# Performance work log

Measured on AMD Instinct MI355X. Metric: run time of the kernel, lower is better.

Reference implementation:

```python
import jax, jax.numpy as jnp
import numpy as np

EMBED_DIM = 768
NUM_HEADS = 12
HEAD_DIM = EMBED_DIM // NUM_HEADS
HIDDEN_DIM = int(EMBED_DIM * 4.0)
LN_EPS = 1e-5


def setup_inputs() -> dict:
    key = jax.random.key(0)
    ks = jax.random.split(key, 8)
    B, N, C = 16, 1024, EMBED_DIM
    s = 0.02
    return {
        "x": jax.random.normal(ks[0], (B, N, C), dtype=jnp.float32),
        "ln1_g": jnp.ones((C,), jnp.float32),
        "ln1_b": jnp.zeros((C,), jnp.float32),
        "qkv_w": jax.random.normal(ks[1], (C, 3 * C), jnp.float32) * s,
        "qkv_b": jnp.zeros((3 * C,), jnp.float32),
        "proj_w": jax.random.normal(ks[2], (C, C), jnp.float32) * s,
        "proj_b": jnp.zeros((C,), jnp.float32),
        "ln2_g": jnp.ones((C,), jnp.float32),
        "ln2_b": jnp.zeros((C,), jnp.float32),
        "fc1_w": jax.random.normal(ks[3], (C, HIDDEN_DIM), jnp.float32) * s,
        "fc1_b": jnp.zeros((HIDDEN_DIM,), jnp.float32),
        "fc2_w": jax.random.normal(ks[4], (HIDDEN_DIM, C), jnp.float32) * s,
        "fc2_b": jnp.zeros((C,), jnp.float32),
    }


def _layernorm(x, g, b):
    mu = jnp.mean(x, axis=-1, keepdims=True)
    var = jnp.mean(jnp.square(x - mu), axis=-1, keepdims=True)
    return (x - mu) * jax.lax.rsqrt(var + LN_EPS) * g + b


def _attention(x, qkv_w, qkv_b, proj_w, proj_b):
    B, N, C = x.shape
    qkv = x @ qkv_w + qkv_b                       # [B,N,3C]
    qkv = qkv.reshape(B, N, 3, NUM_HEADS, HEAD_DIM)
    q, k, v = qkv[:, :, 0], qkv[:, :, 1], qkv[:, :, 2]  # [B,N,H,D]
    scale = HEAD_DIM ** -0.5
    attn = jnp.einsum("bqhd,bkhd->bhqk", q, k) * scale
    attn = jax.nn.softmax(attn, axis=-1)
    out = jnp.einsum("bhqk,bkhd->bqhd", attn, v).reshape(B, N, C)
    return out @ proj_w + proj_b


def reference(x, ln1_g, ln1_b, qkv_w, qkv_b, proj_w, proj_b,
              ln2_g, ln2_b, fc1_w, fc1_b, fc2_w, fc2_b):
    x = x + _attention(_layernorm(x, ln1_g, ln1_b), qkv_w, qkv_b, proj_w, proj_b)
    h = _layernorm(x, ln2_g, ln2_b)
    h = jax.nn.gelu(h @ fc1_w + fc1_b, approximate=False)
    return x + (h @ fc2_w + fc2_b)
```

## Files before the change

kernel.cpp:

```cpp
#include <hip/hip_runtime.h>
#include <math.h>

#define SEQ 1024
#define NH 12
#define CC 768

using short8 = __attribute__((ext_vector_type(8))) short;
using bf16x8 = __attribute__((ext_vector_type(8))) __bf16;
using f32x4  = __attribute__((ext_vector_type(4))) float;

__device__ __forceinline__ unsigned short f2bf(float f){
  unsigned u = __builtin_bit_cast(unsigned, f);
  u += 0x7FFF + ((u >> 16) & 1);
  return (unsigned short)(u >> 16);
}

__device__ __forceinline__ void gload16(const void* g, void* l){
  __builtin_amdgcn_global_load_lds((const __attribute__((address_space(1))) unsigned int*)g,
                                   (__attribute__((address_space(3))) unsigned int*)l, 16, 0, 0);
}
__device__ __forceinline__ bf16x8 lds_frag(const unsigned short* p){
  return __builtin_bit_cast(bf16x8, *(const short8*)p);
}
__device__ __forceinline__ bf16x8 gld_frag(const unsigned short* p){
  return __builtin_bit_cast(bf16x8, *(const short8*)p);
}

__global__ __launch_bounds__(256) void wtrans(const float* __restrict__ W,
                                              unsigned short* __restrict__ Wt,
                                              int K, int N){
  __shared__ float tile[32][33];
  int tx = threadIdx.x & 31, ty = threadIdx.x >> 5;
  int n0 = blockIdx.x * 32, k0 = blockIdx.y * 32;
#pragma unroll
  for (int j = 0; j < 4; j++)
    tile[ty + j*8][tx] = W[(size_t)(k0 + ty + j*8) * N + n0 + tx];
  __syncthreads();
#pragma unroll
  for (int j = 0; j < 4; j++)
    Wt[(size_t)(n0 + ty + j*8) * K + k0 + tx] = f2bf(tile[tx][ty + j*8]);
}

__global__ __launch_bounds__(64) void ln_k(const float* __restrict__ x,
                                           const float* __restrict__ g,
                                           const float* __restrict__ be,
                                           unsigned short* __restrict__ out){
  const int row = blockIdx.x;
  const int lane = threadIdx.x;
  const float* xr = x + (size_t)row * CC;
  float4 v[3];
  float s = 0.f, sq = 0.f;
#pragma unroll
  for (int j = 0; j < 3; j++){
    v[j] = *(const float4*)(xr + lane*4 + j*256);
    s  += v[j].x + v[j].y + v[j].z + v[j].w;
    sq += v[j].x*v[j].x + v[j].y*v[j].y + v[j].z*v[j].z + v[j].w*v[j].w;
  }
#pragma unroll
  for (int d = 1; d < 64; d <<= 1){ s += __shfl_xor(s, d); sq += __shfl_xor(sq, d); }
  float mu = s * (1.0f/CC);
  float var = sq * (1.0f/CC) - mu*mu;
  float rstd = rsqrtf(var + 1e-5f);
  unsigned short* orow = out + (size_t)row * CC;
#pragma unroll
  for (int j = 0; j < 3; j++){
    int cb = lane*4 + j*256;
    float4 gv = *(const float4*)(g + cb);
    float4 bv = *(const float4*)(be + cb);
    ushort4 o;
    o.x = f2bf((v[j].x - mu)*rstd*gv.x + bv.x);
    o.y = f2bf((v[j].y - mu)*rstd*gv.y + bv.y);
    o.z = f2bf((v[j].z - mu)*rstd*gv.z + bv.z);
    o.w = f2bf((v[j].w - mu)*rstd*gv.w + bv.w);
    *(ushort4*)(orow + cb) = o;
  }
}

__global__ __launch_bounds__(256) void vextract(const unsigned short* __restrict__ qkv,
                                                unsigned short* __restrict__ vT){
  __shared__ unsigned short tile[32][33];
  int bh = blockIdx.y;
  int b = bh / NH, h = bh % NH;
  int tt = blockIdx.x & 31, dt = blockIdx.x >> 5;
  int tx = threadIdx.x & 31, ty = threadIdx.x >> 5;
#pragma unroll
  for (int j = 0; j < 4; j++)
    tile[ty + j*8][tx] = qkv[(size_t)(b*SEQ + tt*32 + ty + j*8)*2304 + 1536 + h*64 + dt*32 + tx];
  __syncthreads();
#pragma unroll
  for (int j = 0; j < 4; j++)
    vT[((size_t)bh*64 + dt*32 + ty + j*8)*SEQ + tt*32 + tx] = tile[tx][ty + j*8];
}

template<int MODE>
__global__ __launch_bounds__(256, 2) void gemm_bt(const unsigned short* __restrict__ A,
                                                  const unsigned short* __restrict__ Bt,
                                                  const float* __restrict__ bias,
                                                  const float* __restrict__ resid,
                                                  void* __restrict__ outp,
                                                  int M, int N, int K){
  __shared__ __align__(16) unsigned short As[2][128*32];
  __shared__ __align__(16) unsigned short Bs[2][128*32];
  const int t = threadIdx.x;
  const int lane = t & 63;
  const int w = t >> 6;
  const int wr = w >> 1, wc = w & 1;
  const int l15 = lane & 15, lg = lane >> 4;
  const int mtiles = M >> 7;
  const int bm = blockIdx.x % mtiles;
  const int bn = blockIdx.x / mtiles;
  const unsigned short* Abase = A + (size_t)bm * 128 * K;
  const unsigned short* Bbase = Bt + (size_t)bn * 128 * K;

  f32x4 acc[4][4] = {};
  const int nk = K >> 5;
  int buf = 0;

#pragma unroll
  for (int i = 0; i < 2; i++){
    int idx = i*256 + t; int r = idx >> 2; int s = idx & 3; int ss = s ^ ((r >> 1) & 3);
    gload16(Abase + (size_t)r*K + ss*8, &As[0][idx*8]);
  }
#pragma unroll
  for (int i = 0; i < 2; i++){
    int idx = i*256 + t; int r = idx >> 2; int s = idx & 3; int ss = s ^ ((r >> 1) & 3);
    gload16(Bbase + (size_t)r*K + ss*8, &Bs[0][idx*8]);
  }
  __syncthreads();

  for (int kt = 0; kt < nk; ++kt){
    if (kt + 1 < nk){
      const unsigned short* Ak = Abase + (kt + 1) * 32;
      const unsigned short* Bk = Bbase + (kt + 1) * 32;
#pragma unroll
      for (int i = 0; i < 2; i++){
        int idx = i*256 + t; int r = idx >> 2; int s = idx & 3; int ss = s ^ ((r >> 1) & 3);
        gload16(Ak + (size_t)r*K + ss*8, &As[buf^1][idx*8]);
      }
#pragma unroll
      for (int i = 0; i < 2; i++){
        int idx = i*256 + t; int r = idx >> 2; int s = idx & 3; int ss = s ^ ((r >> 1) & 3);
        gload16(Bk + (size_t)r*K + ss*8, &Bs[buf^1][idx*8]);
      }
    }
    bf16x8 af[4], bfr[4];
#pragma unroll
    for (int m = 0; m < 4; m++){
      int rr = wr*64 + m*16 + l15;
      int s = lg ^ ((rr >> 1) & 3);
      af[m] = lds_frag(&As[buf][rr*32 + s*8]);
    }
#pragma unroll
    for (int n = 0; n < 4; n++){
      int rr = wc*64 + n*16 + l15;
      int s = lg ^ ((rr >> 1) & 3);
      bfr[n] = lds_frag(&Bs[buf][rr*32 + s*8]);
    }
#pragma unroll
    for (int m = 0; m < 4; m++)
#pragma unroll
      for (int n = 0; n < 4; n++)
        acc[m][n] = __builtin_amdgcn_mfma_f32_16x16x32_bf16(af[m], bfr[n], acc[m][n], 0, 0, 0);
    __syncthreads();
    buf ^= 1;
  }

  const int row0 = bm*128 + wr*64 + lg*4;
  const int col0 = bn*128 + wc*64 + l15;
#pragma unroll
  for (int n = 0; n < 4; n++){
    int c = col0 + n*16;
    float bv = bias[c];
#pragma unroll
    for (int m = 0; m < 4; m++){
      int r = row0 + m*16;
#pragma unroll
      for (int i = 0; i < 4; i++){
        size_t idx = (size_t)(r + i) * N + c;
        float v = acc[m][n][i] + bv;
        if constexpr (MODE == 0){
          ((unsigned short*)outp)[idx] = f2bf(v);
        } else if constexpr (MODE == 1){
          ((float*)outp)[idx] = resid[idx] + v;
        } else {
          float gv = 0.5f * v * (1.0f + erff(v * 0.70710678118654752440f));
          ((unsigned short*)outp)[idx] = f2bf(gv);
        }
      }
    }
  }
}

__global__ __launch_bounds__(256, 2) void attn_k(const unsigned short* __restrict__ qkv,
                                                 const unsigned short* __restrict__ vT,
                                                 unsigned short* __restrict__ aout){
  __shared__ __align__(16) unsigned short Ks[2][64*64];
  __shared__ __align__(16) unsigned short Vs[2][64*64];
  __shared__ __align__(16) unsigned short Ps[4][32*64];
  const int t = threadIdx.x, lane = t & 63, w = t >> 6;
  const int l15 = lane & 15, lg = lane >> 4;
  const int qt = blockIdx.x;
  const int bh = blockIdx.y;
  const int b = bh / NH, h = bh % NH;
  const size_t qrow0 = (size_t)b * SEQ + qt*128 + w*32;

  bf16x8 qf[2][2];
#pragma unroll
  for (int nf = 0; nf < 2; nf++)
#pragma unroll
    for (int ks = 0; ks < 2; ks++)
      qf[nf][ks] = gld_frag(qkv + (qrow0 + nf*16 + l15)*2304 + h*64 + ks*32 + lg*8);

  f32x4 o[2][4] = {};
  float mold[2] = {-3.0e38f, -3.0e38f};
  float lsum[2] = {0.f, 0.f};

  const unsigned short* Kgl = qkv + (size_t)b * SEQ * 2304 + 768 + h*64;
  const unsigned short* Vgl = vT + (size_t)bh * 64 * SEQ;

  auto stageKV = [&](int bufi, int kt){
#pragma unroll
    for (int i = 0; i < 2; i++){
      int idx = i*256 + t; int r = idx >> 3; int s = idx & 7; int ss = s ^ (r & 7);
      gload16(Kgl + (size_t)(kt*64 + r)*2304 + ss*8, &Ks[bufi][idx*8]);
    }
#pragma unroll
    for (int i = 0; i < 2; i++){
      int idx = i*256 + t; int r = idx >> 3; int s = idx & 7; int ss = s ^ (r & 7);
      gload16(Vgl + (size_t)r*SEQ + kt*64 + ss*8, &Vs[bufi][idx*8]);
    }
  };

  stageKV(0, 0);
  __syncthreads();
  int buf = 0;

  for (int kt = 0; kt < 16; ++kt){
    if (kt + 1 < 16) stageKV(buf ^ 1, kt + 1);

    f32x4 st[4][2] = {};
#pragma unroll
    for (int ks = 0; ks < 2; ks++){
      bf16x8 kf[4];
#pragma unroll
      for (int mf = 0; mf < 4; mf++){
        int rr = mf*16 + l15;
        int sc = (ks*4 + lg) ^ (rr & 7);
        kf[mf] = lds_frag(&Ks[buf][rr*64 + sc*8]);
      }
#pragma unroll
      for (int mf = 0; mf < 4; mf++)
#pragma unroll
        for (int nf = 0; nf < 2; nf++)
          st[mf][nf] = __builtin_amdgcn_mfma_f32_16x16x32_bf16(kf[mf], qf[nf][ks], st[mf][nf], 0, 0, 0);
    }

    float fsc[2];
#pragma unroll
    for (int nf = 0; nf < 2; nf++){
      float mx = -3.0e38f;
#pragma unroll
      for (int mf = 0; mf < 4; mf++)
#pragma unroll
        for (int i = 0; i < 4; i++){
          float sv = st[mf][nf][i] * 0.125f;
          st[mf][nf][i] = sv;
          mx = fmaxf(mx, sv);
        }
      mx = fmaxf(mx, __shfl_xor(mx, 16));
      mx = fmaxf(mx, __shfl_xor(mx, 32));
      float nm = fmaxf(mold[nf], mx);
      float f = __expf(mold[nf] - nm);
      mold[nf] = nm;
      float rs = 0.f;
#pragma unroll
      for (int mf = 0; mf < 4; mf++)
#pragma unroll
        for (int i = 0; i < 4; i++){
          float p = __expf(st[mf][nf][i] - nm);
          st[mf][nf][i] = p;
          rs += p;
        }
      rs += __shfl_xor(rs, 16);
      rs += __shfl_xor(rs, 32);
      lsum[nf] = lsum[nf]*f + rs;
      fsc[nf] = f;
    }

#pragma unroll
    for (int nf = 0; nf < 2; nf++)
#pragma unroll
      for (int mf = 0; mf < 4; mf++)
#pragma unroll
        for (int i = 0; i < 4; i++){
          int rP = nf*16 + l15;
          int col = mf*16 + lg*4 + i;
          Ps[w][rP*64 + (col ^ ((rP & 7) << 3))] = f2bf(st[mf][nf][i]);
        }

#pragma unroll
    for (int mm = 0; mm < 2; mm++)
#pragma unroll
      for (int i = 0; i < 4; i++){
        float fo = __shfl(fsc[mm], lg*4 + i);
#pragma unroll
        for (int df = 0; df < 4; df++)
          o[mm][df][i] *= fo;
      }

#pragma unroll
    for (int ks = 0; ks < 2; ks++){
      bf16x8 pf[2], vf[4];
#pragma unroll
      for (int mm = 0; mm < 2; mm++){
        int rP = mm*16 + l15;
        int sc = (ks*4 + lg) ^ (rP & 7);
        pf[mm] = lds_frag(&Ps[w][rP*64 + sc*8]);
      }
#pragma unroll
      for (int df = 0; df < 4; df++){
        int rr = df*16 + l15;
        int sc = (ks*4 + lg) ^ (rr & 7);
        vf[df] = lds_frag(&Vs[buf][rr*64 + sc*8]);
      }
#pragma unroll
      for (int mm = 0; mm < 2; mm++)
#pragma unroll
        for (int df = 0; df < 4; df++)
          o[mm][df] = __builtin_amdgcn_mfma_f32_16x16x32_bf16(pf[mm], vf[df], o[mm][df], 0, 0, 0);
    }
    __syncthreads();
    buf ^= 1;
  }

#pragma unroll
  for (int mm = 0; mm < 2; mm++){
    float li = 1.0f / lsum[mm];
#pragma unroll
    for (int i = 0; i < 4; i++){
      float rl = __shfl(li, lg*4 + i);
      size_t r = qrow0 + mm*16 + lg*4 + i;
#pragma unroll
      for (int df = 0; df < 4; df++)
        aout[r*CC + h*64 + df*16 + l15] = f2bf(o[mm][df][i] * rl);
    }
  }
}

extern "C" void kernel_launch(void* const* d_in, const int* in_sizes, int n_in,
                              void* d_out, int out_size, void* d_ws, size_t ws_size,
                              hipStream_t stream){
  (void)in_sizes; (void)n_in; (void)out_size; (void)ws_size;
  const float* x      = (const float*)d_in[0];
  const float* ln1_g  = (const float*)d_in[1];
  const float* ln1_b  = (const float*)d_in[2];
  const float* qkv_w  = (const float*)d_in[3];
  const float* qkv_b  = (const float*)d_in[4];
  const float* proj_w = (const float*)d_in[5];
  const float* proj_b = (const float*)d_in[6];
  const float* ln2_g  = (const float*)d_in[7];
  const float* ln2_b  = (const float*)d_in[8];
  const float* fc1_w  = (const float*)d_in[9];
  const float* fc1_b  = (const float*)d_in[10];
  const float* fc2_w  = (const float*)d_in[11];
  const float* fc2_b  = (const float*)d_in[12];
  float* out = (float*)d_out;
  char* ws = (char*)d_ws;

  unsigned short* ln_out  = (unsigned short*)(ws);
  unsigned short* qkv_buf = (unsigned short*)(ws + 25165824);
  unsigned short* vTb     = (unsigned short*)(ws + 100663296);
  unsigned short* attn    = (unsigned short*)(ws + 125829120);
  unsigned short* hbuf    = qkv_buf;
  char* wbase = ws + 150994944;
  unsigned short* wq = (unsigned short*)(wbase);
  unsigned short* wp = (unsigned short*)(wbase + 3538944);
  unsigned short* w1 = (unsigned short*)(wbase + 4718592);
  unsigned short* w2 = (unsigned short*)(wbase + 9437184);

  wtrans<<<dim3(72, 24), 256, 0, stream>>>(qkv_w, wq, 768, 2304);
  wtrans<<<dim3(24, 24), 256, 0, stream>>>(proj_w, wp, 768, 768);
  wtrans<<<dim3(96, 24), 256, 0, stream>>>(fc1_w, w1, 768, 3072);
  wtrans<<<dim3(24, 96), 256, 0, stream>>>(fc2_w, w2, 3072, 768);

  ln_k<<<16384, 64, 0, stream>>>(x, ln1_g, ln1_b, ln_out);
  gemm_bt<0><<<128*18, 256, 0, stream>>>(ln_out, wq, qkv_b, nullptr, qkv_buf, 16384, 2304, 768);
  vextract<<<dim3(64, 192), 256, 0, stream>>>(qkv_buf, vTb);
  attn_k<<<dim3(8, 192), 256, 0, stream>>>(qkv_buf, vTb, attn);
  gemm_bt<1><<<128*6, 256, 0, stream>>>(attn, wp, proj_b, x, out, 16384, 768, 768);
  ln_k<<<16384, 64, 0, stream>>>(out, ln2_g, ln2_b, ln_out);
  gemm_bt<2><<<128*24, 256, 0, stream>>>(ln_out, w1, fc1_b, nullptr, hbuf, 16384, 3072, 768);
  gemm_bt<1><<<128*6, 256, 0, stream>>>(hbuf, w2, fc2_b, out, out, 16384, 768, 3072);
}
```

Baseline: 625.4 us.

## Replace GEMM with 256x256-tile 8-wave pipelined kernel and tanh-based GELU

```diff
diff --git a/kernel.cpp b/kernel.cpp
--- a/kernel.cpp
+++ b/kernel.cpp
@@ -93,86 +93,157 @@
 }
 
 template<int MODE>
-__global__ __launch_bounds__(256, 2) void gemm_bt(const unsigned short* __restrict__ A,
+__global__ __launch_bounds__(512, 2) void gemm256(const unsigned short* __restrict__ A,
                                                   const unsigned short* __restrict__ Bt,
                                                   const float* __restrict__ bias,
                                                   const float* __restrict__ resid,
                                                   void* __restrict__ outp,
                                                   int M, int N, int K){
-  __shared__ __align__(16) unsigned short As[2][128*32];
-  __shared__ __align__(16) unsigned short Bs[2][128*32];
+  __shared__ __align__(16) unsigned short lds[2][4][128*64];
   const int t = threadIdx.x;
-  const int lane = t & 63;
-  const int w = t >> 6;
-  const int wr = w >> 1, wc = w & 1;
+  const int lane = t & 63, w = t >> 6;
+  const int wr = w >> 2, wc = w & 3;
   const int l15 = lane & 15, lg = lane >> 4;
-  const int mtiles = M >> 7;
-  const int bm = blockIdx.x % mtiles;
-  const int bn = blockIdx.x / mtiles;
-  const unsigned short* Abase = A + (size_t)bm * 128 * K;
-  const unsigned short* Bbase = Bt + (size_t)bn * 128 * K;
-
-  f32x4 acc[4][4] = {};
-  const int nk = K >> 5;
-  int buf = 0;
-
-#pragma unroll
-  for (int i = 0; i < 2; i++){
-    int idx = i*256 + t; int r = idx >> 2; int s = idx & 3; int ss = s ^ ((r >> 1) & 3);
-    gload16(Abase + (size_t)r*K + ss*8, &As[0][idx*8]);
-  }
-#pragma unroll
-  for (int i = 0; i < 2; i++){
-    int idx = i*256 + t; int r = idx >> 2; int s = idx & 3; int ss = s ^ ((r >> 1) & 3);
-    gload16(Bbase + (size_t)r*K + ss*8, &Bs[0][idx*8]);
-  }
-  __syncthreads();
-
+  const int mtiles = M >> 8;
+  const int cpx = gridDim.x >> 3;
+  const int bid = blockIdx.x;
+  const int swz = (bid & 7) * cpx + (bid >> 3);
+  const int bm = swz % mtiles, bn = swz / mtiles;
+
+  const unsigned short* gA0 = A  + (size_t)bm*256*K;
+  const unsigned short* gA1 = gA0 + (size_t)128*K;
+  const unsigned short* gB0 = Bt + (size_t)bn*256*K;
+  const unsigned short* gB1 = gB0 + (size_t)128*K;
+
+  const int csw = (t & 7) ^ ((t >> 3) & 7);
+  const size_t off0 = (size_t)(t >> 3)*K + csw*8;
+  const size_t off1 = off0 + (size_t)64*K;
+
+  auto stageh = [&](int bi, int rg, const unsigned short* gb, int kt){
+    const unsigned short* s = gb + (size_t)kt*64;
+    unsigned short* d = &lds[bi][rg][0];
+    gload16(s + off0, d + t*8);
+    gload16(s + off1, d + 4096 + t*8);
+  };
+
+  const int cx0 = (lg ^ (l15 & 7)) * 8;
+  const int cx1 = ((4 + lg) ^ (l15 & 7)) * 8;
+  const int rB = (wc & 1)*64 + l15;
+
+  f32x4 acc[8][4] = {};
+  const int nk = K >> 6;
+
+  stageh(0,0,gA0,0); stageh(0,1,gA1,0); stageh(0,2,gB0,0); stageh(0,3,gB1,0);
+  stageh(1,0,gA0,1); stageh(1,1,gA1,1); stageh(1,2,gB0,1);
+  asm volatile("s_waitcnt vmcnt(6)" ::: "memory");
+  __builtin_amdgcn_sched_barrier(0);
+  __builtin_amdgcn_s_barrier();
+
+  bf16x8 afr[8][2], bfl[2][2], bfh[2][2];
   for (int kt = 0; kt < nk; ++kt){
-    if (kt + 1 < nk){
-      const unsigned short* Ak = Abase + (kt + 1) * 32;
-      const unsigned short* Bk = Bbase + (kt + 1) * 32;
-#pragma unroll
-      for (int i = 0; i < 2; i++){
-        int idx = i*256 + t; int r = idx >> 2; int s = idx & 3; int ss = s ^ ((r >> 1) & 3);
-        gload16(Ak + (size_t)r*K + ss*8, &As[buf^1][idx*8]);
-      }
-#pragma unroll
-      for (int i = 0; i < 2; i++){
-        int idx = i*256 + t; int r = idx >> 2; int s = idx & 3; int ss = s ^ ((r >> 1) & 3);
-        gload16(Bk + (size_t)r*K + ss*8, &Bs[buf^1][idx*8]);
-      }
-    }
-    bf16x8 af[4], bfr[4];
+    const int buf = kt & 1;
+    const unsigned short* pA = &lds[buf][wr][0];
+    const unsigned short* pB = &lds[buf][2 + (wc >> 1)][0];
+
 #pragma unroll
     for (int m = 0; m < 4; m++){
-      int rr = wr*64 + m*16 + l15;
-      int s = lg ^ ((rr >> 1) & 3);
-      af[m] = lds_frag(&As[buf][rr*32 + s*8]);
-    }
-#pragma unroll
-    for (int n = 0; n < 4; n++){
-      int rr = wc*64 + n*16 + l15;
-      int s = lg ^ ((rr >> 1) & 3);
-      bfr[n] = lds_frag(&Bs[buf][rr*32 + s*8]);
-    }
+      afr[m][0] = lds_frag(pA + (m*16 + l15)*64 + cx0);
+      afr[m][1] = lds_frag(pA + (m*16 + l15)*64 + cx1);
+    }
+#pragma unroll
+    for (int n = 0; n < 2; n++){
+      bfl[n][0] = lds_frag(pB + (rB + n*16)*64 + cx0);
+      bfl[n][1] = lds_frag(pB + (rB + n*16)*64 + cx1);
+    }
+#pragma unroll
+    for (int m = 4; m < 8; m++){
+      afr[m][0] = lds_frag(pA + (m*16 + l15)*64 + cx0);
+      afr[m][1] = lds_frag(pA + (m*16 + l15)*64 + cx1);
+    }
+    if (kt + 1 < nk) stageh((kt+1)&1, 3, gB1, kt+1);
+    __builtin_amdgcn_sched_barrier(0);
+    __builtin_amdgcn_s_barrier();
+    asm volatile("s_waitcnt lgkmcnt(8)" ::: "memory");
+    __builtin_amdgcn_sched_barrier(0);
+    __builtin_amdgcn_s_setprio(1);
 #pragma unroll
     for (int m = 0; m < 4; m++)
 #pragma unroll
-      for (int n = 0; n < 4; n++)
-        acc[m][n] = __builtin_amdgcn_mfma_f32_16x16x32_bf16(af[m], bfr[n], acc[m][n], 0, 0, 0);
-    __syncthreads();
-    buf ^= 1;
-  }
-
-  const int row0 = bm*128 + wr*64 + lg*4;
-  const int col0 = bn*128 + wc*64 + l15;
+      for (int n = 0; n < 2; n++){
+        acc[m][n] = __builtin_amdgcn_mfma_f32_16x16x32_bf16(afr[m][0], bfl[n][0], acc[m][n], 0,0,0);
+        acc[m][n] = __builtin_amdgcn_mfma_f32_16x16x32_bf16(afr[m][1], bfl[n][1], acc[m][n], 0,0,0);
+      }
+    __builtin_amdgcn_s_setprio(0);
+    __builtin_amdgcn_sched_barrier(0);
+    __builtin_amdgcn_s_barrier();
+
+#pragma unroll
+    for (int n = 0; n < 2; n++){
+      bfh[n][0] = lds_frag(pB + (rB + (n+2)*16)*64 + cx0);
+      bfh[n][1] = lds_frag(pB + (rB + (n+2)*16)*64 + cx1);
+    }
+    if (kt + 2 < nk) stageh(buf, 0, gA0, kt+2);
+    __builtin_amdgcn_sched_barrier(0);
+    __builtin_amdgcn_s_barrier();
+    asm volatile("s_waitcnt lgkmcnt(4)" ::: "memory");
+    __builtin_amdgcn_sched_barrier(0);
+    __builtin_amdgcn_s_setprio(1);
+#pragma unroll
+    for (int m = 4; m < 8; m++)
+#pragma unroll
+      for (int n = 0; n < 2; n++){
+        acc[m][n] = __builtin_amdgcn_mfma_f32_16x16x32_bf16(afr[m][0], bfl[n][0], acc[m][n], 0,0,0);
+        acc[m][n] = __builtin_amdgcn_mfma_f32_16x16x32_bf16(afr[m][1], bfl[n][1], acc[m][n], 0,0,0);
+      }
+    __builtin_amdgcn_s_setprio(0);
+    __builtin_amdgcn_sched_barrier(0);
+    __builtin_amdgcn_s_barrier();
+
+    if (kt + 2 < nk) stageh(buf, 1, gA1, kt+2);
+    __builtin_amdgcn_sched_barrier(0);
+    __builtin_amdgcn_s_barrier();
+    asm volatile("s_waitcnt lgkmcnt(0)" ::: "memory");
+    __builtin_amdgcn_sched_barrier(0);
+    __builtin_amdgcn_s_setprio(1);
+#pragma unroll
+    for (int m = 4; m < 8; m++)
+#pragma unroll
+      for (int n = 0; n < 2; n++){
+        acc[m][n+2] = __builtin_amdgcn_mfma_f32_16x16x32_bf16(afr[m][0], bfh[n][0], acc[m][n+2], 0,0,0);
+        acc[m][n+2] = __builtin_amdgcn_mfma_f32_16x16x32_bf16(afr[m][1], bfh[n][1], acc[m][n+2], 0,0,0);
+      }
+    __builtin_amdgcn_s_setprio(0);
+    __builtin_amdgcn_sched_barrier(0);
+    __builtin_amdgcn_s_barrier();
+
+    if (kt + 2 < nk) stageh(buf, 2, gB0, kt+2);
+    __builtin_amdgcn_sched_barrier(0);
+    __builtin_amdgcn_s_barrier();
+    __builtin_amdgcn_s_setprio(1);
+#pragma unroll
+    for (int m = 0; m < 4; m++)
+#pragma unroll
+      for (int n = 0; n < 2; n++){
+        acc[m][n+2] = __builtin_amdgcn_mfma_f32_16x16x32_bf16(afr[m][0], bfh[n][0], acc[m][n+2], 0,0,0);
+        acc[m][n+2] = __builtin_amdgcn_mfma_f32_16x16x32_bf16(afr[m][1], bfh[n][1], acc[m][n+2], 0,0,0);
+      }
+    __builtin_amdgcn_s_setprio(0);
+    if (kt < nk - 1){
+      if (kt + 2 < nk) { asm volatile("s_waitcnt vmcnt(6)" ::: "memory"); }
+      else             { asm volatile("s_waitcnt vmcnt(0)" ::: "memory"); }
+    }
+    __builtin_amdgcn_sched_barrier(0);
+    __builtin_amdgcn_s_barrier();
+  }
+
+  const int row0 = bm*256 + wr*128 + lg*4;
+  const int col0 = bn*256 + wc*64 + l15;
 #pragma unroll
   for (int n = 0; n < 4; n++){
     int c = col0 + n*16;
     float bv = bias[c];
 #pragma unroll
-    for (int m = 0; m < 4; m++){
+    for (int m = 0; m < 8; m++){
       int r = row0 + m*16;
 #pragma unroll
       for (int i = 0; i < 4; i++){
@@ -183,7 +254,10 @@
         } else if constexpr (MODE == 1){
           ((float*)outp)[idx] = resid[idx] + v;
         } else {
-          float gv = 0.5f * v * (1.0f + erff(v * 0.70710678118654752440f));
+          float u = v + 0.044715f*v*v*v;
+          float a = fminf(-1.5957691216057308f*u, 80.f);
+          float e = __expf(a);
+          float gv = 0.5f*v*(1.0f + (1.f - e)/(1.f + e));
           ((unsigned short*)outp)[idx] = f2bf(gv);
         }
       }
@@ -384,11 +458,11 @@
   wtrans<<<dim3(24, 96), 256, 0, stream>>>(fc2_w, w2, 3072, 768);
 
   ln_k<<<16384, 64, 0, stream>>>(x, ln1_g, ln1_b, ln_out);
-  gemm_bt<0><<<128*18, 256, 0, stream>>>(ln_out, wq, qkv_b, nullptr, qkv_buf, 16384, 2304, 768);
+  gemm256<0><<<64*9, 512, 0, stream>>>(ln_out, wq, qkv_b, nullptr, qkv_buf, 16384, 2304, 768);
   vextract<<<dim3(64, 192), 256, 0, stream>>>(qkv_buf, vTb);
   attn_k<<<dim3(8, 192), 256, 0, stream>>>(qkv_buf, vTb, attn);
-  gemm_bt<1><<<128*6, 256, 0, stream>>>(attn, wp, proj_b, x, out, 16384, 768, 768);
+  gemm256<1><<<64*3, 512, 0, stream>>>(attn, wp, proj_b, x, out, 16384, 768, 768);
   ln_k<<<16384, 64, 0, stream>>>(out, ln2_g, ln2_b, ln_out);
-  gemm_bt<2><<<128*24, 256, 0, stream>>>(ln_out, w1, fc1_b, nullptr, hbuf, 16384, 3072, 768);
-  gemm_bt<1><<<128*6, 256, 0, stream>>>(hbuf, w2, fc2_b, out, out, 16384, 768, 3072);
-}
+  gemm256<2><<<64*12, 512, 0, stream>>>(ln_out, w1, fc1_b, nullptr, hbuf, 16384, 3072, 768);
+  gemm256<1><<<64*3, 512, 0, stream>>>(hbuf, w2, fc2_b, out, out, 16384, 768, 3072);
+}
```

Result: no change. 635.1 us (+1.5%).
